# Performance work log

Hardware: AMD Instinct MI355X
Metric: run time of the kernel (lower is better)

Reference implementation:

```python
import jax, jax.numpy as jnp
import numpy as np

TOP_K = 2
B, S, H, I, E = 1, 2048, 1024, 4096, 8


def setup_inputs() -> dict:
    key = jax.random.key(0)
    k1, k2, k3, k4 = jax.random.split(key, 4)
    x = jax.random.normal(k1, (B, S, H), dtype=jnp.float32)
    gate_w = jax.random.normal(k2, (E, H), dtype=jnp.float32)
    w1 = jax.random.normal(k3, (E, I, H), dtype=jnp.float32)
    w2 = jax.random.normal(k4, (E, H, I), dtype=jnp.float32)
    return {"x": x, "gate_w": gate_w, "w1": w1, "w2": w2}


def reference(x, gate_w, w1, w2):
    b, s, h = x.shape
    xf = x.reshape(-1, h)                      # [T, H]
    T = xf.shape[0]
    logits = xf @ gate_w.T                     # [T, E]
    probs = jax.nn.softmax(logits, axis=-1)
    wts, idx = jax.lax.top_k(probs, TOP_K)     # [T, k]
    wts = wts / jnp.sum(wts, axis=-1, keepdims=True)
    # combine[t, e] = routing weight of expert e for token t (0 if not selected)
    combine = jnp.zeros((T, w1.shape[0]), dtype=x.dtype)
    combine = combine.at[jnp.arange(T)[:, None], idx].add(wts)
    # dense dispatch: every expert processes every token, masked/weighted by combine
    hid = jax.nn.silu(jnp.einsum('th,eih->tei', xf, w1))   # [T, E, I]
    y = jnp.einsum('tei,ehi->teh', hid, w2)                # [T, E, H]
    out = jnp.einsum('teh,te->th', y, combine)             # [T, H]
    return out.reshape(b, s, h)
```

## Files before the change

### kernel.cpp

```cpp
#include <hip/hip_runtime.h>
#include <stdint.h>

#define TT 2048
#define HH 1024
#define II 4096
#define EE 8
#define KS 4
#define KSPAN (II / KS)

typedef __attribute__((ext_vector_type(4))) float floatx4;
typedef __attribute__((ext_vector_type(8))) __bf16 bf16x8;

__device__ __forceinline__ unsigned short f2bf(float f) {
  union { float f; unsigned u; } v; v.f = f;
  return (unsigned short)((v.u + 0x7FFFu + ((v.u >> 16) & 1u)) >> 16);
}

__device__ __forceinline__ void async_ld16(const void* g, void* l) {
  __builtin_amdgcn_global_load_lds(
      (__attribute__((address_space(1))) void*)g,
      (__attribute__((address_space(3))) void*)l, 16, 0, 0);
}

#define CFENCE asm volatile("" ::: "memory")
#define WAIT_VM0 asm volatile("s_waitcnt vmcnt(0)" ::: "memory")

__global__ __launch_bounds__(256) void k_convw(
    const float* __restrict__ w1, const float* __restrict__ w2,
    unsigned short* __restrict__ w1b, unsigned short* __restrict__ w2b) {
  const int N4 = EE * II * HH / 4;
  int idx = blockIdx.x * 256 + threadIdx.x;
  const int stride = gridDim.x * 256;
  for (int i = idx; i < 2 * N4; i += stride) {
    const float* src;
    unsigned short* dst;
    int j;
    if (i < N4) { src = w1; dst = w1b; j = i; }
    else        { src = w2; dst = w2b; j = i - N4; }
    floatx4 a = ((const floatx4*)src)[j];
    ushort4 o;
    o.x = f2bf(a.x); o.y = f2bf(a.y); o.z = f2bf(a.z); o.w = f2bf(a.w);
    ((ushort4*)dst)[j] = o;
  }
}

__global__ __launch_bounds__(256) void k_gating(
    const float* __restrict__ x, const float* __restrict__ gw,
    unsigned short* __restrict__ xb, int* __restrict__ sel_e,
    float* __restrict__ sel_w, int* __restrict__ counts) {
  int t = blockIdx.x;
  int tid = threadIdx.x;
  floatx4 xv = ((const floatx4*)(x + (size_t)t * HH))[tid];
  ushort4 xo;
  xo.x = f2bf(xv.x); xo.y = f2bf(xv.y); xo.z = f2bf(xv.z); xo.w = f2bf(xv.w);
  ((ushort4*)(xb + (size_t)t * HH))[tid] = xo;

  float part[EE];
#pragma unroll
  for (int e = 0; e < EE; e++) {
    floatx4 g = ((const floatx4*)(gw + e * HH))[tid];
    part[e] = xv.x * g.x + xv.y * g.y + xv.z * g.z + xv.w * g.w;
  }
#pragma unroll
  for (int e = 0; e < EE; e++) {
    float v = part[e];
#pragma unroll
    for (int off = 32; off > 0; off >>= 1) v += __shfl_down(v, off, 64);
    part[e] = v;
  }
  __shared__ float red[4][EE];
  int wave = tid >> 6;
  if ((tid & 63) == 0) {
#pragma unroll
    for (int e = 0; e < EE; e++) red[wave][e] = part[e];
  }
  __syncthreads();
  if (tid == 0) {
    float lg[EE];
#pragma unroll
    for (int e = 0; e < EE; e++)
      lg[e] = red[0][e] + red[1][e] + red[2][e] + red[3][e];
    int e0 = 0;
#pragma unroll
    for (int e = 1; e < EE; e++) if (lg[e] > lg[e0]) e0 = e;
    int e1 = (e0 == 0) ? 1 : 0;
#pragma unroll
    for (int e = 0; e < EE; e++) if (e != e0 && lg[e] > lg[e1]) e1 = e;
    float w0 = 1.f / (1.f + expf(lg[e1] - lg[e0]));
    sel_e[t * 2] = e0; sel_e[t * 2 + 1] = e1;
    sel_w[t * 2] = w0; sel_w[t * 2 + 1] = 1.f - w0;
    atomicAdd(&counts[e0], 1);
    atomicAdd(&counts[e1], 1);
  }
}

__global__ __launch_bounds__(256) void k_fill(
    const int* __restrict__ counts, const int* __restrict__ sel_e,
    const float* __restrict__ sel_w, int* __restrict__ bases,
    int* __restrict__ row_token, float* __restrict__ row_w,
    int* __restrict__ inv_slot) {
  __shared__ int lb[EE];
  __shared__ int lc[EE];
  int tid = threadIdx.x;
  if (tid == 0) {
    int s = 0;
    for (int e = 0; e < EE; e++) { lb[e] = s; s += counts[e]; }
  }
  if (tid < EE) lc[tid] = 0;
  __syncthreads();
  for (int p = tid; p < TT * 2; p += 256) {
    int e = sel_e[p];
    int slot = lb[e] + atomicAdd(&lc[e], 1);
    row_token[slot] = p >> 1;
    row_w[slot] = sel_w[p];
    inv_slot[p] = slot;
  }
  __syncthreads();
  if (tid < EE) bases[tid] = lb[tid];
}

__global__ __launch_bounds__(256) void k_gemm1(
    const unsigned short* __restrict__ xb,
    const unsigned short* __restrict__ w1b,
    unsigned short* __restrict__ hid,
    const int* __restrict__ counts, const int* __restrict__ bases,
    const int* __restrict__ row_token) {
  const int e = blockIdx.z;
  const int count = counts[e];
  const int m0 = blockIdx.y * 128;
  if (m0 >= count) return;
  const int n0 = blockIdx.x * 128;
  const int base = bases[e];

  __shared__ __align__(16) unsigned short Smem[4 * 4096];
  unsigned short* const A0b = Smem;
  unsigned short* const A1b = Smem + 4096;
  unsigned short* const B0b = Smem + 8192;
  unsigned short* const B1b = Smem + 12288;

  const int tid = threadIdx.x;
  const int lane = tid & 63;
  const int wave = tid >> 6;
  const int wm = (wave & 1) * 64;
  const int wn = (wave >> 1) * 64;
  const int quad = lane >> 4;
  const int l16 = lane & 15;

  const int rA0 = tid >> 2;
  const int swz = (tid & 3) ^ ((tid >> 3) & 3);
  const int cc = swz * 8;
  const int ldsOff = tid * 8;

  int g0 = m0 + rA0;      if (g0 > count - 1) g0 = count - 1;
  int g1 = m0 + rA0 + 64; if (g1 > count - 1) g1 = count - 1;
  const unsigned short* aS0 = xb + (size_t)row_token[base + g0] * HH + cc;
  const unsigned short* aS1 = xb + (size_t)row_token[base + g1] * HH + cc;
  const unsigned short* wp = w1b + (size_t)e * II * HH;
  const unsigned short* bS0 = wp + (size_t)(n0 + rA0) * HH + cc;
  const unsigned short* bS1 = bS0 + (size_t)64 * HH;

  int offA[4], offB[4];
#pragma unroll
  for (int i = 0; i < 4; i++) {
    const int Ra = wm + i * 16 + l16;
    offA[i] = Ra * 32 + 8 * (quad ^ ((Ra >> 1) & 3));
    const int Rb = wn + i * 16 + l16;
    offB[i] = Rb * 32 + 8 * (quad ^ ((Rb >> 1) & 3));
  }

  const floatx4 fz = {0.f, 0.f, 0.f, 0.f};
  floatx4 acc[4][4];
#pragma unroll
  for (int i = 0; i < 4; i++)
#pragma unroll
    for (int j = 0; j < 4; j++) acc[i][j] = fz;

  async_ld16(aS0, A0b + ldsOff);
  async_ld16(aS1, A0b + ldsOff + 2048);
  async_ld16(bS0, B0b + ldsOff);
  async_ld16(bS1, B0b + ldsOff + 2048);
  WAIT_VM0;
  __builtin_amdgcn_s_barrier();
  CFENCE;

  unsigned short* Ac = A0b; unsigned short* An = A1b;
  unsigned short* Bc = B0b; unsigned short* Bn = B1b;

  for (int k0 = 0; k0 < HH; k0 += 32) {
    if (k0 + 32 < HH) {
      async_ld16(aS0 + k0 + 32, An + ldsOff);
      async_ld16(aS1 + k0 + 32, An + ldsOff + 2048);
      async_ld16(bS0 + k0 + 32, Bn + ldsOff);
      async_ld16(bS1 + k0 + 32, Bn + ldsOff + 2048);
    }
    CFENCE;
    bf16x8 af[4], bfr[4];
#pragma unroll
    for (int i = 0; i < 4; i++) {
      af[i]  = *(const bf16x8*)(Ac + offA[i]);
      bfr[i] = *(const bf16x8*)(Bc + offB[i]);
    }
#pragma unroll
    for (int i = 0; i < 4; i++)
#pragma unroll
      for (int j = 0; j < 4; j++)
        acc[i][j] = __builtin_amdgcn_mfma_f32_16x16x32_bf16(af[i], bfr[j], acc[i][j], 0, 0, 0);
    WAIT_VM0;
    __builtin_amdgcn_s_barrier();
    CFENCE;
    { unsigned short* t = Ac; Ac = An; An = t; }
    { unsigned short* t = Bc; Bc = Bn; Bn = t; }
  }

  unsigned short* Sl = Smem + wave * (16 * 72);
#pragma unroll
  for (int i = 0; i < 4; i++) {
#pragma unroll
    for (int r = 0; r < 4; r++) {
      const int row16 = quad * 4 + r;
#pragma unroll
      for (int j = 0; j < 4; j++) {
        float z = acc[i][j][r];
        Sl[row16 * 72 + l16 + 16 * j] = f2bf(z / (1.f + __expf(-z)));
      }
    }
#pragma unroll
    for (int half = 0; half < 2; half++) {
      const int row16 = (lane >> 3) + 8 * half;
      const int m = wm + i * 16 + row16;
      if (m0 + m < count) {
        bf16x8 v = *(const bf16x8*)(Sl + row16 * 72 + (lane & 7) * 8);
        *(bf16x8*)(hid + (size_t)(base + m0 + m) * II + n0 + wn + (lane & 7) * 8) = v;
      }
    }
  }
}

__global__ __launch_bounds__(256) void k_gemm2(
    const unsigned short* __restrict__ hid,
    const unsigned short* __restrict__ w2b,
    float* __restrict__ yp,
    const int* __restrict__ counts, const int* __restrict__ bases) {
  const int e = blockIdx.z;
  const int count = counts[e];
  const int m0 = blockIdx.y * 128;
  if (m0 >= count) return;
  const int nt = blockIdx.x & 7;
  const int ks = blockIdx.x >> 3;
  const int n0 = nt * 128;
  const int base = bases[e];
  const int kbeg = ks * KSPAN;

  __shared__ __align__(16) unsigned short Smem2[4 * 4096];
  unsigned short* const A0b = Smem2;
  unsigned short* const A1b = Smem2 + 4096;
  unsigned short* const B0b = Smem2 + 8192;
  unsigned short* const B1b = Smem2 + 12288;

  const int tid = threadIdx.x;
  const int lane = tid & 63;
  const int wave = tid >> 6;
  const int wm = (wave & 1) * 64;
  const int wn = (wave >> 1) * 64;
  const int quad = lane >> 4;
  const int l16 = lane & 15;

  const int rA0 = tid >> 2;
  const int swz = (tid & 3) ^ ((tid >> 3) & 3);
  const int cc = swz * 8;
  const int ldsOff = tid * 8;

  int g0 = m0 + rA0;      if (g0 > count - 1) g0 = count - 1;
  int g1 = m0 + rA0 + 64; if (g1 > count - 1) g1 = count - 1;
  const unsigned short* aS0 = hid + (size_t)(base + g0) * II + kbeg + cc;
  const unsigned short* aS1 = hid + (size_t)(base + g1) * II + kbeg + cc;
  const unsigned short* wp = w2b + (size_t)e * HH * II;
  const unsigned short* bS0 = wp + (size_t)(n0 + rA0) * II + kbeg + cc;
  const unsigned short* bS1 = bS0 + (size_t)64 * II;

  int offA[4], offB[4];
#pragma unroll
  for (int i = 0; i < 4; i++) {
    const int Ra = wm + i * 16 + l16;
    offA[i] = Ra * 32 + 8 * (quad ^ ((Ra >> 1) & 3));
    const int Rb = wn + i * 16 + l16;
    offB[i] = Rb * 32 + 8 * (quad ^ ((Rb >> 1) & 3));
  }

  const floatx4 fz = {0.f, 0.f, 0.f, 0.f};
  floatx4 acc[4][4];
#pragma unroll
  for (int i = 0; i < 4; i++)
#pragma unroll
    for (int j = 0; j < 4; j++) acc[i][j] = fz;

  async_ld16(aS0, A0b + ldsOff);
  async_ld16(aS1, A0b + ldsOff + 2048);
  async_ld16(bS0, B0b + ldsOff);
  async_ld16(bS1, B0b + ldsOff + 2048);
  WAIT_VM0;
  __builtin_amdgcn_s_barrier();
  CFENCE;

  unsigned short* Ac = A0b; unsigned short* An = A1b;
  unsigned short* Bc = B0b; unsigned short* Bn = B1b;

  for (int k0 = 0; k0 < KSPAN; k0 += 32) {
    if (k0 + 32 < KSPAN) {
      async_ld16(aS0 + k0 + 32, An + ldsOff);
      async_ld16(aS1 + k0 + 32, An + ldsOff + 2048);
      async_ld16(bS0 + k0 + 32, Bn + ldsOff);
      async_ld16(bS1 + k0 + 32, Bn + ldsOff + 2048);
    }
    CFENCE;
    bf16x8 af[4], bfr[4];
#pragma unroll
    for (int i = 0; i < 4; i++) {
      af[i]  = *(const bf16x8*)(Ac + offA[i]);
      bfr[i] = *(const bf16x8*)(Bc + offB[i]);
    }
#pragma unroll
    for (int i = 0; i < 4; i++)
#pragma unroll
      for (int j = 0; j < 4; j++)
        acc[i][j] = __builtin_amdgcn_mfma_f32_16x16x32_bf16(af[i], bfr[j], acc[i][j], 0, 0, 0);
    WAIT_VM0;
    __builtin_amdgcn_s_barrier();
    CFENCE;
    { unsigned short* t = Ac; Ac = An; An = t; }
    { unsigned short* t = Bc; Bc = Bn; Bn = t; }
  }

#pragma unroll
  for (int i = 0; i < 4; i++) {
#pragma unroll
    for (int r = 0; r < 4; r++) {
      const int m = wm + i * 16 + quad * 4 + r;
      if (m0 + m < count) {
        float* op = yp + ((size_t)ks * (TT * 2) + base + m0 + m) * HH + n0 + wn + l16;
#pragma unroll
        for (int j = 0; j < 4; j++) op[j * 16] = acc[i][j][r];
      }
    }
  }
}

__global__ __launch_bounds__(256) void k_combine(
    const float* __restrict__ yp, const int* __restrict__ inv_slot,
    const float* __restrict__ sel_w, float* __restrict__ out) {
  const int t = blockIdx.x;
  const int tid = threadIdx.x;
  const int s0 = inv_slot[2 * t];
  const int s1 = inv_slot[2 * t + 1];
  const float w0 = sel_w[2 * t];
  const float w1 = sel_w[2 * t + 1];
  floatx4 a = {0.f, 0.f, 0.f, 0.f};
  floatx4 b = {0.f, 0.f, 0.f, 0.f};
#pragma unroll
  for (int ks = 0; ks < KS; ks++) {
    a += ((const floatx4*)(yp + ((size_t)ks * (TT * 2) + s0) * HH))[tid];
    b += ((const floatx4*)(yp + ((size_t)ks * (TT * 2) + s1) * HH))[tid];
  }
  floatx4 v = w0 * a + w1 * b;
  ((floatx4*)(out + (size_t)t * HH))[tid] = v;
}

extern "C" void kernel_launch(void* const* d_in, const int* in_sizes, int n_in,
                              void* d_out, int out_size, void* d_ws, size_t ws_size,
                              hipStream_t stream) {
  const float* x  = (const float*)d_in[0];
  const float* gw = (const float*)d_in[1];
  const float* w1 = (const float*)d_in[2];
  const float* w2 = (const float*)d_in[3];
  float* out = (float*)d_out;

  char* ws = (char*)d_ws;
  size_t off = 0;
  auto take = [&](size_t n) -> char* {
    char* p = ws + off;
    off += (n + 255) & ~(size_t)255;
    return p;
  };
  unsigned short* xb  = (unsigned short*)take((size_t)TT * HH * 2);
  unsigned short* hid = (unsigned short*)take((size_t)TT * 2 * II * 2);
  unsigned short* w1b = (unsigned short*)take((size_t)EE * II * HH * 2);
  float* yp = (float*)w1b;
  unsigned short* w2b = (unsigned short*)take((size_t)EE * II * HH * 2);
  int*   counts    = (int*)take(EE * 4);
  int*   bases     = (int*)take(EE * 4);
  int*   row_token = (int*)take((size_t)TT * 2 * 4);
  float* row_w     = (float*)take((size_t)TT * 2 * 4);
  int*   sel_e     = (int*)take((size_t)TT * 2 * 4);
  float* sel_w     = (float*)take((size_t)TT * 2 * 4);
  int*   inv_slot  = (int*)take((size_t)TT * 2 * 4);
  if (off > ws_size) return;

  hipMemsetAsync(counts, 0, EE * 4, stream);

  k_convw<<<2048, 256, 0, stream>>>(w1, w2, w1b, w2b);
  k_gating<<<TT, 256, 0, stream>>>(x, gw, xb, sel_e, sel_w, counts);
  k_fill<<<1, 256, 0, stream>>>(counts, sel_e, sel_w, bases, row_token, row_w, inv_slot);
  k_gemm1<<<dim3(II / 128, 16, EE), 256, 0, stream>>>(xb, w1b, hid, counts, bases, row_token);
  k_gemm2<<<dim3(8 * KS, 16, EE), 256, 0, stream>>>(hid, w2b, yp, counts, bases);
  k_combine<<<TT, 256, 0, stream>>>(yp, inv_slot, sel_w, out);
}
```

Baseline: 502.2 us.

## Triple-buffer GEMM LDS pipeline and fuse weight conversion with gating kernel

Both grouped GEMM kernels move from double to triple buffering of LDS tiles, prefetching two K-steps ahead and waiting with vmcnt(4) instead of draining all loads each iteration. The weight fp32->bf16 conversion and the gating kernel are merged into one launch, with the conversion part using nontemporal 32-byte loads and 16-byte stores. The aim is to hide global-load latency in the GEMMs and cut one launch plus the conversion's memory traffic overhead. LDS per block rises from 32KB to 48KB, which may reduce occupancy.

```diff
diff --git a/kernel.cpp b/kernel.cpp
--- a/kernel.cpp
+++ b/kernel.cpp
@@ -10,6 +10,7 @@
 
 typedef __attribute__((ext_vector_type(4))) float floatx4;
 typedef __attribute__((ext_vector_type(8))) __bf16 bf16x8;
+typedef __attribute__((ext_vector_type(8))) unsigned short ushort8v;
 
 __device__ __forceinline__ unsigned short f2bf(float f) {
   union { float f; unsigned u; } v; v.f = f;
@@ -23,33 +24,38 @@
 }
 
 #define CFENCE asm volatile("" ::: "memory")
-#define WAIT_VM0 asm volatile("s_waitcnt vmcnt(0)" ::: "memory")
-
-__global__ __launch_bounds__(256) void k_convw(
+#define WAIT_VM(n) asm volatile("s_waitcnt vmcnt(" #n ")" ::: "memory")
+
+__global__ __launch_bounds__(256) void k_prep(
+    const float* __restrict__ x, const float* __restrict__ gw,
     const float* __restrict__ w1, const float* __restrict__ w2,
-    unsigned short* __restrict__ w1b, unsigned short* __restrict__ w2b) {
-  const int N4 = EE * II * HH / 4;
-  int idx = blockIdx.x * 256 + threadIdx.x;
-  const int stride = gridDim.x * 256;
-  for (int i = idx; i < 2 * N4; i += stride) {
-    const float* src;
-    unsigned short* dst;
-    int j;
-    if (i < N4) { src = w1; dst = w1b; j = i; }
-    else        { src = w2; dst = w2b; j = i - N4; }
-    floatx4 a = ((const floatx4*)src)[j];
-    ushort4 o;
-    o.x = f2bf(a.x); o.y = f2bf(a.y); o.z = f2bf(a.z); o.w = f2bf(a.w);
-    ((ushort4*)dst)[j] = o;
-  }
-}
-
-__global__ __launch_bounds__(256) void k_gating(
-    const float* __restrict__ x, const float* __restrict__ gw,
-    unsigned short* __restrict__ xb, int* __restrict__ sel_e,
+    unsigned short* __restrict__ xb, unsigned short* __restrict__ w1b,
+    unsigned short* __restrict__ w2b, int* __restrict__ sel_e,
     float* __restrict__ sel_w, int* __restrict__ counts) {
-  int t = blockIdx.x;
-  int tid = threadIdx.x;
+  const int bid = blockIdx.x;
+  const int tid = threadIdx.x;
+
+  if (bid >= TT) {
+    const int cb = bid - TT;
+    const int tensor = cb >> 11;
+    const int b = cb & 2047;
+    const float* src = tensor ? w2 : w1;
+    unsigned short* dst = tensor ? w2b : w1b;
+    const int idx = b * 256 + tid;
+#pragma unroll
+    for (int it = 0; it < 8; ++it) {
+      const int c = idx + it * 524288;
+      floatx4 a = __builtin_nontemporal_load((const floatx4*)src + 2 * c);
+      floatx4 bb = __builtin_nontemporal_load((const floatx4*)src + 2 * c + 1);
+      ushort8v o;
+      o[0] = f2bf(a.x); o[1] = f2bf(a.y); o[2] = f2bf(a.z); o[3] = f2bf(a.w);
+      o[4] = f2bf(bb.x); o[5] = f2bf(bb.y); o[6] = f2bf(bb.z); o[7] = f2bf(bb.w);
+      ((ushort8v*)dst)[c] = o;
+    }
+    return;
+  }
+
+  const int t = bid;
   floatx4 xv = ((const floatx4*)(x + (size_t)t * HH))[tid];
   ushort4 xo;
   xo.x = f2bf(xv.x); xo.y = f2bf(xv.y); xo.z = f2bf(xv.z); xo.w = f2bf(xv.w);
@@ -132,11 +138,7 @@
   const int n0 = blockIdx.x * 128;
   const int base = bases[e];
 
-  __shared__ __align__(16) unsigned short Smem[4 * 4096];
-  unsigned short* const A0b = Smem;
-  unsigned short* const A1b = Smem + 4096;
-  unsigned short* const B0b = Smem + 8192;
-  unsigned short* const B1b = Smem + 12288;
+  __shared__ __align__(16) unsigned short Smem[3 * 8192];
 
   const int tid = threadIdx.x;
   const int lane = tid & 63;
@@ -165,7 +167,7 @@
     const int Ra = wm + i * 16 + l16;
     offA[i] = Ra * 32 + 8 * (quad ^ ((Ra >> 1) & 3));
     const int Rb = wn + i * 16 + l16;
-    offB[i] = Rb * 32 + 8 * (quad ^ ((Rb >> 1) & 3));
+    offB[i] = 4096 + Rb * 32 + 8 * (quad ^ ((Rb >> 1) & 3));
   }
 
   const floatx4 fz = {0.f, 0.f, 0.f, 0.f};
@@ -175,41 +177,47 @@
 #pragma unroll
     for (int j = 0; j < 4; j++) acc[i][j] = fz;
 
-  async_ld16(aS0, A0b + ldsOff);
-  async_ld16(aS1, A0b + ldsOff + 2048);
-  async_ld16(bS0, B0b + ldsOff);
-  async_ld16(bS1, B0b + ldsOff + 2048);
-  WAIT_VM0;
+  unsigned short* b0 = Smem;
+  unsigned short* b1 = Smem + 8192;
+  unsigned short* b2 = Smem + 16384;
+
+  async_ld16(aS0, b0 + ldsOff);
+  async_ld16(aS1, b0 + ldsOff + 2048);
+  async_ld16(bS0, b0 + 4096 + ldsOff);
+  async_ld16(bS1, b0 + 4096 + ldsOff + 2048);
+  async_ld16(aS0 + 32, b1 + ldsOff);
+  async_ld16(aS1 + 32, b1 + ldsOff + 2048);
+  async_ld16(bS0 + 32, b1 + 4096 + ldsOff);
+  async_ld16(bS1 + 32, b1 + 4096 + ldsOff + 2048);
+  WAIT_VM(4);
   __builtin_amdgcn_s_barrier();
   CFENCE;
 
-  unsigned short* Ac = A0b; unsigned short* An = A1b;
-  unsigned short* Bc = B0b; unsigned short* Bn = B1b;
-
   for (int k0 = 0; k0 < HH; k0 += 32) {
-    if (k0 + 32 < HH) {
-      async_ld16(aS0 + k0 + 32, An + ldsOff);
-      async_ld16(aS1 + k0 + 32, An + ldsOff + 2048);
-      async_ld16(bS0 + k0 + 32, Bn + ldsOff);
-      async_ld16(bS1 + k0 + 32, Bn + ldsOff + 2048);
+    const bool issue2 = (k0 + 64 < HH);
+    if (issue2) {
+      async_ld16(aS0 + k0 + 64, b2 + ldsOff);
+      async_ld16(aS1 + k0 + 64, b2 + ldsOff + 2048);
+      async_ld16(bS0 + k0 + 64, b2 + 4096 + ldsOff);
+      async_ld16(bS1 + k0 + 64, b2 + 4096 + ldsOff + 2048);
     }
     CFENCE;
     bf16x8 af[4], bfr[4];
 #pragma unroll
     for (int i = 0; i < 4; i++) {
-      af[i]  = *(const bf16x8*)(Ac + offA[i]);
-      bfr[i] = *(const bf16x8*)(Bc + offB[i]);
+      af[i]  = *(const bf16x8*)(b0 + offA[i]);
+      bfr[i] = *(const bf16x8*)(b0 + offB[i]);
     }
 #pragma unroll
     for (int i = 0; i < 4; i++)
 #pragma unroll
       for (int j = 0; j < 4; j++)
         acc[i][j] = __builtin_amdgcn_mfma_f32_16x16x32_bf16(af[i], bfr[j], acc[i][j], 0, 0, 0);
-    WAIT_VM0;
+    CFENCE;
+    if (issue2) { WAIT_VM(4); } else { WAIT_VM(0); }
     __builtin_amdgcn_s_barrier();
     CFENCE;
-    { unsigned short* t = Ac; Ac = An; An = t; }
-    { unsigned short* t = Bc; Bc = Bn; Bn = t; }
+    unsigned short* t = b0; b0 = b1; b1 = b2; b2 = t;
   }
 
   unsigned short* Sl = Smem + wave * (16 * 72);
@@ -251,11 +259,7 @@
   const int base = bases[e];
   const int kbeg = ks * KSPAN;
 
-  __shared__ __align__(16) unsigned short Smem2[4 * 4096];
-  unsigned short* const A0b = Smem2;
-  unsigned short* const A1b = Smem2 + 4096;
-  unsigned short* const B0b = Smem2 + 8192;
-  unsigned short* const B1b = Smem2 + 12288;
+  __shared__ __align__(16) unsigned short Smem2[3 * 8192];
 
   const int tid = threadIdx.x;
   const int lane = tid & 63;
@@ -284,7 +288,7 @@
     const int Ra = wm + i * 16 + l16;
     offA[i] = Ra * 32 + 8 * (quad ^ ((Ra >> 1) & 3));
     const int Rb = wn + i * 16 + l16;
-    offB[i] = Rb * 32 + 8 * (quad ^ ((Rb >> 1) & 3));
+    offB[i] = 4096 + Rb * 32 + 8 * (quad ^ ((Rb >> 1) & 3));
   }
 
   const floatx4 fz = {0.f, 0.f, 0.f, 0.f};
@@ -294,41 +298,47 @@
 #pragma unroll
     for (int j = 0; j < 4; j++) acc[i][j] = fz;
 
-  async_ld16(aS0, A0b + ldsOff);
-  async_ld16(aS1, A0b + ldsOff + 2048);
-  async_ld16(bS0, B0b + ldsOff);
-  async_ld16(bS1, B0b + ldsOff + 2048);
-  WAIT_VM0;
+  unsigned short* b0 = Smem2;
+  unsigned short* b1 = Smem2 + 8192;
+  unsigned short* b2 = Smem2 + 16384;
+
+  async_ld16(aS0, b0 + ldsOff);
+  async_ld16(aS1, b0 + ldsOff + 2048);
+  async_ld16(bS0, b0 + 4096 + ldsOff);
+  async_ld16(bS1, b0 + 4096 + ldsOff + 2048);
+  async_ld16(aS0 + 32, b1 + ldsOff);
+  async_ld16(aS1 + 32, b1 + ldsOff + 2048);
+  async_ld16(bS0 + 32, b1 + 4096 + ldsOff);
+  async_ld16(bS1 + 32, b1 + 4096 + ldsOff + 2048);
+  WAIT_VM(4);
   __builtin_amdgcn_s_barrier();
   CFENCE;
 
-  unsigned short* Ac = A0b; unsigned short* An = A1b;
-  unsigned short* Bc = B0b; unsigned short* Bn = B1b;
-
   for (int k0 = 0; k0 < KSPAN; k0 += 32) {
-    if (k0 + 32 < KSPAN) {
-      async_ld16(aS0 + k0 + 32, An + ldsOff);
-      async_ld16(aS1 + k0 + 32, An + ldsOff + 2048);
-      async_ld16(bS0 + k0 + 32, Bn + ldsOff);
-      async_ld16(bS1 + k0 + 32, Bn + ldsOff + 2048);
+    const bool issue2 = (k0 + 64 < KSPAN);
+    if (issue2) {
+      async_ld16(aS0 + k0 + 64, b2 + ldsOff);
+      async_ld16(aS1 + k0 + 64, b2 + ldsOff + 2048);
+      async_ld16(bS0 + k0 + 64, b2 + 4096 + ldsOff);
+      async_ld16(bS1 + k0 + 64, b2 + 4096 + ldsOff + 2048);
     }
     CFENCE;
     bf16x8 af[4], bfr[4];
 #pragma unroll
     for (int i = 0; i < 4; i++) {
-      af[i]  = *(const bf16x8*)(Ac + offA[i]);
-      bfr[i] = *(const bf16x8*)(Bc + offB[i]);
+      af[i]  = *(const bf16x8*)(b0 + offA[i]);
+      bfr[i] = *(const bf16x8*)(b0 + offB[i]);
     }
 #pragma unroll
     for (int i = 0; i < 4; i++)
 #pragma unroll
       for (int j = 0; j < 4; j++)
         acc[i][j] = __builtin_amdgcn_mfma_f32_16x16x32_bf16(af[i], bfr[j], acc[i][j], 0, 0, 0);
-    WAIT_VM0;
+    CFENCE;
+    if (issue2) { WAIT_VM(4); } else { WAIT_VM(0); }
     __builtin_amdgcn_s_barrier();
     CFENCE;
-    { unsigned short* t = Ac; Ac = An; An = t; }
-    { unsigned short* t = Bc; Bc = Bn; Bn = t; }
+    unsigned short* t = b0; b0 = b1; b1 = b2; b2 = t;
   }
 
 #pragma unroll
@@ -397,8 +407,7 @@
 
   hipMemsetAsync(counts, 0, EE * 4, stream);
 
-  k_convw<<<2048, 256, 0, stream>>>(w1, w2, w1b, w2b);
-  k_gating<<<TT, 256, 0, stream>>>(x, gw, xb, sel_e, sel_w, counts);
+  k_prep<<<TT + 4096, 256, 0, stream>>>(x, gw, w1, w2, xb, w1b, w2b, sel_e, sel_w, counts);
   k_fill<<<1, 256, 0, stream>>>(counts, sel_e, sel_w, bases, row_token, row_w, inv_slot);
   k_gemm1<<<dim3(II / 128, 16, EE), 256, 0, stream>>>(xb, w1b, hid, counts, bases, row_token);
   k_gemm2<<<dim3(8 * KS, 16, EE), 256, 0, stream>>>(hid, w2b, yp, counts, bases);
```

Result: faster. 477.2 us (-5.0%).
